# Optimization experiments

Hardware: AMD Instinct MI355X
Metric: run time of the kernel (lower is better)

## Reference

```python
import jax, jax.numpy as jnp
import numpy as np

EPS = 1e-8


def _conv1d(x, w, b):
    # x: [B, E, L], w: [F, E, K], b: [F] -> [B, F, L] (k=3, pad=1 keeps length)
    y = jax.lax.conv_general_dilated(
        x, w, window_strides=(1,), padding=[(1, 1)],
        dimension_numbers=("NCH", "OIH", "NCH"))
    return y + b[None, :, None]


def setup_inputs() -> dict:
    key = jax.random.key(0)
    kq, ka, ke, kw, kb, ku = jax.random.split(key, 6)
    B, QL, AL = 512, 128, 512
    V, E, F, K = 50000, 300, 400, 3
    question = jax.random.randint(kq, (B, QL), 0, V + 1, dtype=jnp.int64)
    answer = jax.random.randint(ka, (B, AL), 0, V + 1, dtype=jnp.int64)
    emb_table = jax.random.normal(ke, (V + 1, E), dtype=jnp.float32)
    emb_table = emb_table.at[0].set(0.0)  # padding_idx=0
    conv_w = jax.random.normal(kw, (F, E, K), dtype=jnp.float32) * 0.05
    conv_b = jax.random.normal(kb, (F,), dtype=jnp.float32) * 0.05
    U = jax.random.normal(ku, (F, F), dtype=jnp.float32) * 0.1
    return {"question": question, "answer": answer, "emb_table": emb_table,
            "conv_w": conv_w, "conv_b": conv_b, "U": U}


def reference(question, answer, emb_table, conv_w, conv_b, U):
    q = emb_table[question]              # [B, QL, E]
    a = emb_table[answer]                # [B, AL, E]
    Q = _conv1d(q.transpose(0, 2, 1), conv_w, conv_b)   # [B, F, QL]
    A = _conv1d(a.transpose(0, 2, 1), conv_w, conv_b)   # [B, F, AL]
    # G = tanh(Q^T U A): [B, QL, AL]
    G = jnp.tanh(jnp.einsum("bfq,fg,bga->bqa", Q, U, A))
    roQ = jax.nn.softmax(jnp.max(G, axis=2), axis=1)    # [B, QL]
    roA = jax.nn.softmax(jnp.max(G, axis=1), axis=1)    # [B, AL]
    rQ = jnp.einsum("bfq,bq->bf", Q, roQ)               # [B, F]
    rA = jnp.einsum("bfa,ba->bf", A, roA)               # [B, F]
    nQ = jnp.maximum(jnp.linalg.norm(rQ, axis=1), EPS)
    nA = jnp.maximum(jnp.linalg.norm(rA, axis=1), EPS)
    return jnp.sum(rQ * rA, axis=1) / (nQ * nA)         # [B]
```

## Files before the change

kernel.cpp:

```cpp
#include <hip/hip_runtime.h>
#include <math.h>

typedef unsigned int   uint32;
typedef unsigned short ushort16;
typedef __attribute__((ext_vector_type(8))) short  short8;
typedef __attribute__((ext_vector_type(4))) float  floatx4;

#define Bb   512
#define QLn  128
#define ALn  512
#define En   300
#define Fn   400
#define OW   416
#define EPAD 320
#define NV   50001
#define ECROWS 50176
#define ECSTRIDE 2560

typedef const __attribute__((address_space(1))) unsigned int guint_t;
typedef __attribute__((address_space(3))) unsigned int luint_t;
#define GLDS16(g, l) __builtin_amdgcn_global_load_lds((guint_t*)(g), (luint_t*)(l), 16, 0, 0)

static __device__ __forceinline__ float bf_lo(uint32 u) { return __uint_as_float(u << 16); }
static __device__ __forceinline__ float bf_hi(uint32 u) { return __uint_as_float(u & 0xffff0000u); }
static __device__ __forceinline__ ushort16 f2bf(float f) {
    uint32 u = __float_as_uint(f);
    uint32 r = (u + 0x7fffu + ((u >> 16) & 1u)) >> 16;
    return (ushort16)r;
}
static __device__ __forceinline__ uint32 pack2(float a, float b) {
    return (uint32)f2bf(a) | ((uint32)f2bf(b) << 16);
}

__global__ __launch_bounds__(128) void embcvt_kernel(
        const float* __restrict__ emb, char* __restrict__ embbf)
{
    const int r = blockIdx.x, j = threadIdx.x;
    const float* er = emb + (size_t)r * En;
    uint32* orow = (uint32*)(embbf + (size_t)r * 640);
    for (int d = j; d < 160; d += 128) {
        uint32 v = 0;
        if (d < 150) {
            float2 f2v = *(const float2*)(er + 2 * d);
            v = pack2(f2v.x, f2v.y);
        }
        orow[d] = v;
    }
}

__global__ __launch_bounds__(256) void prep_wt(
        const float* __restrict__ W, const float* __restrict__ cb,
        ushort16* __restrict__ Wt2, float* __restrict__ bias2)
{
    const int f = blockIdx.x, t = threadIdx.x;
    for (int p2 = t; p2 < 480; p2 += 256) {
        int p = 2 * p2;
        float v0 = 0.f, v1 = 0.f;
        if (f < Fn) {
            int kk = p / EPAD, e = p - kk * EPAD;
            if (e < En)     v0 = W[(size_t)f * 900 + e * 3 + kk];
            if (e + 1 < En) v1 = W[(size_t)f * 900 + (e + 1) * 3 + kk];
        }
        *(uint32*)&Wt2[(size_t)f * 960 + p] = pack2(v0, v1);
    }
    if (t == 0) bias2[f] = (f < Fn) ? cb[f] : 0.f;
}

__global__ __launch_bounds__(256) void prep_ub(
        const float* __restrict__ U, ushort16* __restrict__ Ub)
{
    const int g = blockIdx.x, t = threadIdx.x;
    uint32* orow = (uint32*)(Ub + (size_t)g * 416);
    for (int f2 = t; f2 < 208; f2 += 256) {
        int f = 2 * f2;
        float v0 = 0.f, v1 = 0.f;
        if (g < Fn) {
            if (f < Fn)     v0 = U[(size_t)f * Fn + g];
            if (f + 1 < Fn) v1 = U[(size_t)(f + 1) * Fn + g];
        }
        orow[f2] = pack2(v0, v1);
    }
}

__global__ __launch_bounds__(512) void ec_gemm(
        const char* __restrict__ embbf, const char* __restrict__ Wt2,
        char* __restrict__ EC)
{
    __shared__ __align__(16) char As[32768];
    __shared__ __align__(16) char Bs[32768];
    const int t = threadIdx.x, lane = t & 63, w = t >> 6;
    const int v0 = blockIdx.x * 256, c0 = blockIdx.y * 256;
    const int wr = w >> 2, wc = w & 3;
    const int fm = lane & 15;
    const int cg = ((lane & 3) - ((lane >> 3) & 3)) & 3;
    const int rl = lane >> 2;
    const int chunkOff = (((lane >> 4) + (fm >> 1)) & 3) * 16;

    const char* srcA[2];
    const char* srcB[2];
#pragma unroll
    for (int i = 0; i < 2; ++i) {
        srcA[i] = embbf + (size_t)(v0 + w * 32 + i * 16 + rl) * 640 + cg * 16;
        int n = c0 + w * 32 + i * 16 + rl;
        int kk = n / 416, f = n - kk * 416;
        if (n >= 1248) { kk = 0; f = 508; }
        srcB[i] = Wt2 + (size_t)f * 1920 + kk * 640 + cg * 16;
    }
    char* AsW = As + w * 2048;
    char* BsW = Bs + w * 2048;

    floatx4 acc[8][4];
    const floatx4 zz = {0.f, 0.f, 0.f, 0.f};
#pragma unroll
    for (int m = 0; m < 8; ++m)
#pragma unroll
        for (int n = 0; n < 4; ++n) acc[m][n] = zz;

#define ESTG(ko, buf) do {                                                    \
        const int _ko = (ko); const int _bo = (buf) * 16384;                  \
        GLDS16(srcA[0] + _ko, AsW + _bo);                                     \
        GLDS16(srcA[1] + _ko, AsW + _bo + 1024);                              \
        GLDS16(srcB[0] + _ko, BsW + _bo);                                     \
        GLDS16(srcB[1] + _ko, BsW + _bo + 1024);                              \
    } while (0)

    int cur = 0;
    ESTG(0, 0);
    __syncthreads();
    for (int ks = 0; ks < 10; ++ks) {
        const int nxt = cur ^ 1;
        if (ks < 9) ESTG((ks + 1) * 64, nxt);
        short8 af[8], bfv[4];
        const char* Ac = As + cur * 16384;
        const char* Bc = Bs + cur * 16384;
#pragma unroll
        for (int m = 0; m < 8; ++m)
            af[m] = *(const short8*)(Ac + (wr * 128 + m * 16 + fm) * 64 + chunkOff);
#pragma unroll
        for (int n = 0; n < 4; ++n)
            bfv[n] = *(const short8*)(Bc + (wc * 64 + n * 16 + fm) * 64 + chunkOff);
        __builtin_amdgcn_s_setprio(1);
#pragma unroll
        for (int m = 0; m < 8; ++m)
#pragma unroll
            for (int n = 0; n < 4; ++n)
                acc[m][n] = __builtin_amdgcn_mfma_f32_16x16x32_bf16(
                    bfv[n], af[m], acc[m][n], 0, 0, 0);
        __builtin_amdgcn_s_setprio(0);
        __syncthreads();
        cur = nxt;
    }
#undef ESTG

#pragma unroll
    for (int m = 0; m < 8; ++m) {
        const int v = v0 + wr * 128 + m * 16 + fm;
#pragma unroll
        for (int n = 0; n < 4; ++n) {
            const int f0 = c0 + wc * 64 + n * 16 + ((lane >> 4) * 4);
            uint2 o;
            o.x = pack2(acc[m][n][0], acc[m][n][1]);
            o.y = pack2(acc[m][n][2], acc[m][n][3]);
            *(uint2*)(EC + (size_t)v * ECSTRIDE + f0 * 2) = o;
        }
    }
}

static __device__ __forceinline__ void gather_one(
        const int* __restrict__ toks, const char* __restrict__ EC,
        const float* __restrict__ bias2, char* __restrict__ outb,
        int id, int L)
{
    const uint32 uid = (uint32)id;
    const int c = (int)(uid % 52u);
    const int r = (int)(uid / 52u);
    const int l = r & (L - 1), b = r / L;
    const int* tr = toks + (size_t)b * L;
    const int t0 = (l > 0)     ? tr[l - 1] : 0;
    const int t1 = tr[l];
    const int t2 = (l < L - 1) ? tr[l + 1] : 0;
    const uint4 x0 = *(const uint4*)(EC + (size_t)t0 * ECSTRIDE +        c * 16);
    const uint4 x1 = *(const uint4*)(EC + (size_t)t1 * ECSTRIDE +  832 + c * 16);
    const uint4 x2 = *(const uint4*)(EC + (size_t)t2 * ECSTRIDE + 1664 + c * 16);
    const float4 b0 = *(const float4*)(bias2 + c * 8);
    const float4 b1 = *(const float4*)(bias2 + c * 8 + 4);
    uint4 o;
    o.x = pack2(bf_lo(x0.x) + bf_lo(x1.x) + bf_lo(x2.x) + b0.x,
                bf_hi(x0.x) + bf_hi(x1.x) + bf_hi(x2.x) + b0.y);
    o.y = pack2(bf_lo(x0.y) + bf_lo(x1.y) + bf_lo(x2.y) + b0.z,
                bf_hi(x0.y) + bf_hi(x1.y) + bf_hi(x2.y) + b0.w);
    o.z = pack2(bf_lo(x0.z) + bf_lo(x1.z) + bf_lo(x2.z) + b1.x,
                bf_hi(x0.z) + bf_hi(x1.z) + bf_hi(x2.z) + b1.y);
    o.w = pack2(bf_lo(x0.w) + bf_lo(x1.w) + bf_lo(x2.w) + b1.z,
                bf_hi(x0.w) + bf_hi(x1.w) + bf_hi(x2.w) + b1.w);
    *(uint4*)(outb + (size_t)r * 832 + c * 16) = o;
}

#define GQB 1024
#define GAB 4096
__global__ __launch_bounds__(256) void gather_both(
        const int* __restrict__ question, const int* __restrict__ answer,
        const char* __restrict__ EC, const float* __restrict__ bias2,
        char* __restrict__ qb, char* __restrict__ ab, int nb)
{
    const int bx = blockIdx.x, t = threadIdx.x;
    if (bx < GQB) {
        const int total = nb * QLn * 52;
        for (int id = bx * 256 + t; id < total; id += GQB * 256)
            gather_one(question, EC, bias2, qb, id, QLn);
    } else {
        const int total = nb * ALn * 52;
        for (int id = (bx - GQB) * 256 + t; id < total; id += GAB * 256)
            gather_one(answer, EC, bias2, ab, id, ALn);
    }
}

template<int NWM, int NWN, int MF, int NF, int BR>
static __device__ __forceinline__ void qp_tile(
        const char* __restrict__ Qb, const char* __restrict__ Ub,
        char* __restrict__ ob, int col0, char* As, char* Bs)
{
    const int t = threadIdx.x, lane = t & 63, w = t >> 6;
    const int wr = w / NWN, wc = w % NWN;
    const int fm = lane & 15;
    const int cg = ((lane & 3) - ((lane >> 3) & 3)) & 3;
    const int rl = lane >> 2;
    const int chunkOff = (((lane >> 4) + (fm >> 1)) & 3) * 16;

    const char* srcA = Qb + (size_t)(w * 16 + rl) * 832 + cg * 16;
    const char* srcB0; const char* srcB1 = 0;
    if (BR == 256) {
        srcB0 = Ub + (size_t)(col0 + w * 32 + rl) * 832 + cg * 16;
        srcB1 = srcB0 + (size_t)16 * 832;
    } else {
        srcB0 = Ub + (size_t)(col0 + w * 16 + rl) * 832 + cg * 16;
        srcB1 = Ub + (size_t)(col0 + 128 + w * 16 + rl) * 832 + cg * 16;
    }
    char* AsW = As + w * 1024;
    char* BsW0; char* BsW1;
    if (BR == 256) { BsW0 = Bs + w * 2048; BsW1 = BsW0 + 1024; }
    else           { BsW0 = Bs + w * 1024; BsW1 = Bs + 8192 + w * 1024; }
    const int BUFB = BR * 64;

    floatx4 acc[MF][NF];
    const floatx4 zz = {0.f, 0.f, 0.f, 0.f};
#pragma unroll
    for (int m = 0; m < MF; ++m)
#pragma unroll
        for (int n = 0; n < NF; ++n) acc[m][n] = zz;

#define QSTG(ko, buf) do {                                                    \
        const int _ko = (ko);                                                 \
        GLDS16(srcA + _ko, AsW + (buf) * 8192);                               \
        GLDS16(srcB0 + _ko, BsW0 + (buf) * BUFB);                             \
        if (BR == 256 || w < 2) GLDS16(srcB1 + _ko, BsW1 + (buf) * BUFB);     \
    } while (0)

    int cur = 0;
    QSTG(0, 0);
    __syncthreads();
    for (int ks = 0; ks < 13; ++ks) {
        const int nxt = cur ^ 1;
        if (ks < 12) QSTG((ks + 1) * 64, nxt);
        short8 af[MF], bfv[NF];
        const char* Ac = As + cur * 8192;
        const char* Bc = Bs + cur * BUFB;
#pragma unroll
        for (int m = 0; m < MF; ++m)
            af[m] = *(const short8*)(Ac + (wr * (MF * 16) + m * 16 + fm) * 64 + chunkOff);
#pragma unroll
        for (int n = 0; n < NF; ++n)
            bfv[n] = *(const short8*)(Bc + (wc * (NF * 16) + n * 16 + fm) * 64 + chunkOff);
        __builtin_amdgcn_s_setprio(1);
#pragma unroll
        for (int m = 0; m < MF; ++m)
#pragma unroll
            for (int n = 0; n < NF; ++n)
                acc[m][n] = __builtin_amdgcn_mfma_f32_16x16x32_bf16(
                    af[m], bfv[n], acc[m][n], 0, 0, 0);
        __builtin_amdgcn_s_setprio(0);
        __syncthreads();
        cur = nxt;
    }
#undef QSTG

#pragma unroll
    for (int m = 0; m < MF; ++m) {
        const int row = wr * (MF * 16) + m * 16 + ((lane >> 4) * 4);
#pragma unroll
        for (int n = 0; n < NF; ++n) {
            const int col = col0 + wc * (NF * 16) + n * 16 + fm;
#pragma unroll
            for (int r = 0; r < 4; ++r)
                *(ushort16*)(ob + (size_t)(row + r) * 832 + col * 2) =
                    f2bf(acc[m][n][r]);
        }
    }
}

__global__ __launch_bounds__(512) void qp_gemm(
        const char* __restrict__ qb, const char* __restrict__ Ub,
        char* __restrict__ qpb, int nb)
{
    __shared__ __align__(16) char As[16384];
    __shared__ __align__(16) char Bs[32768];
    const int bx = blockIdx.x;
    const int xcd = bx & 7, rest = bx >> 3;
    const int nt = rest & 1, b = (rest >> 1) * 8 + xcd;
    if (b >= nb) return;
    const char* Qb = qb + (size_t)b * 106496;
    char* ob = qpb + (size_t)b * 106496;
    if (nt == 0)
        qp_tile<2, 4, 4, 4, 256>(Qb, Ub, ob, 0, As, Bs);
    else
        qp_tile<4, 2, 2, 5, 160>(Qb, Ub, ob, 256, As, Bs);
}

__global__ __launch_bounds__(256) void fused_g(
        const ushort16* __restrict__ Qp,
        const ushort16* __restrict__ Av,
        float* __restrict__ rowPart,
        float* __restrict__ colMg,
        int nb)
{
    __shared__ __align__(16) char Qs[16384];
    __shared__ __align__(16) char Asl[32768];
    __shared__ float rowM4[128][4];

    const int t = threadIdx.x, lane = t & 63, w = t >> 6;
    const int bx = blockIdx.x;
    const int xcd = bx & 7, rest = bx >> 3;
    const int c = rest & 1, b = (rest >> 1) * 8 + xcd;
    if (b >= nb) return;
    const int fm = lane & 15;
    const int cg = ((lane & 3) - ((lane >> 3) & 3)) & 3;
    const int rl = lane >> 2;
    const int chunkOff = (((lane >> 4) + (fm >> 1)) & 3) * 16;

    const char* Qpb = (const char*)Qp + (size_t)b * 106496;
    const char* Ab  = (const char*)Av + (size_t)b * 425984 + (size_t)c * 212992;
    const char* srcQ0 = Qpb + (size_t)(w * 16 + rl) * 832 + cg * 16;
    const char* srcQ1 = Qpb + (size_t)(64 + w * 16 + rl) * 832 + cg * 16;
    const char* srcA0 = Ab  + (size_t)(w * 64 + rl) * 832 + cg * 16;

    floatx4 acc[8][4];
    const floatx4 zz = {0.f, 0.f, 0.f, 0.f};
#pragma unroll
    for (int m = 0; m < 8; ++m)
#pragma unroll
        for (int n = 0; n < 4; ++n) acc[m][n] = zz;

#define FSTG(ko, buf) do {                                                    \
        const int _ko = (ko);                                                 \
        GLDS16(srcQ0 + _ko, Qs + (buf) * 8192 + w * 1024);                    \
        GLDS16(srcQ1 + _ko, Qs + (buf) * 8192 + 4096 + w * 1024);             \
        GLDS16(srcA0 + _ko,         Asl + (buf) * 16384 + w * 4096);          \
        GLDS16(srcA0 + 13312 + _ko, Asl + (buf) * 16384 + w * 4096 + 1024);   \
        GLDS16(srcA0 + 26624 + _ko, Asl + (buf) * 16384 + w * 4096 + 2048);   \
        GLDS16(srcA0 + 39936 + _ko, Asl + (buf) * 16384 + w * 4096 + 3072);   \
    } while (0)

    int cur = 0;
    FSTG(0, 0);
    __syncthreads();

    for (int ks = 0; ks < 13; ++ks) {
        const int nxt = cur ^ 1;
        if (ks < 12) FSTG((ks + 1) * 64, nxt);

        short8 qa[8], aa_[4];
        const char* Qc = Qs + cur * 8192;
        const char* Ac = Asl + cur * 16384;
#pragma unroll
        for (int m = 0; m < 8; ++m)
            qa[m] = *(const short8*)(Qc + (m * 16 + fm) * 64 + chunkOff);
#pragma unroll
        for (int n = 0; n < 4; ++n)
            aa_[n] = *(const short8*)(Ac + (w * 64 + n * 16 + fm) * 64 + chunkOff);
        __builtin_amdgcn_s_setprio(1);
#pragma unroll
        for (int m = 0; m < 8; ++m)
#pragma unroll
            for (int n = 0; n < 4; ++n)
                acc[m][n] = __builtin_amdgcn_mfma_f32_16x16x32_bf16(
                    qa[m], aa_[n], acc[m][n], 0, 0, 0);
        __builtin_amdgcn_s_setprio(0);
        __syncthreads();
        cur = nxt;
    }
#undef FSTG

#pragma unroll
    for (int m = 0; m < 8; ++m)
#pragma unroll
        for (int r = 0; r < 4; ++r) {
            float v = fmaxf(fmaxf(acc[m][0][r], acc[m][1][r]),
                            fmaxf(acc[m][2][r], acc[m][3][r]));
            v = fmaxf(v, __shfl_xor(v, 1));
            v = fmaxf(v, __shfl_xor(v, 2));
            v = fmaxf(v, __shfl_xor(v, 4));
            v = fmaxf(v, __shfl_xor(v, 8));
            if (fm == 0) rowM4[m * 16 + (lane >> 4) * 4 + r][w] = v;
        }
#pragma unroll
    for (int n = 0; n < 4; ++n) {
        float v = -1e30f;
#pragma unroll
        for (int m = 0; m < 8; ++m)
#pragma unroll
            for (int r = 0; r < 4; ++r) v = fmaxf(v, acc[m][n][r]);
        v = fmaxf(v, __shfl_xor(v, 16));
        v = fmaxf(v, __shfl_xor(v, 32));
        if (lane < 16)
            colMg[(size_t)b * 512 + c * 256 + w * 64 + n * 16 + lane] = v;
    }
    __syncthreads();
    if (t < 128)
        rowPart[((size_t)b * 2 + c) * 128 + t] =
            fmaxf(fmaxf(rowM4[t][0], rowM4[t][1]),
                  fmaxf(rowM4[t][2], rowM4[t][3]));
}

static __device__ __forceinline__ float block_reduce_max_1k(float v, volatile float* red) {
    int t = threadIdx.x;
    red[t] = v; __syncthreads();
    for (int s = 512; s > 0; s >>= 1) {
        if (t < s) red[t] = fmaxf(red[t], red[t + s]);
        __syncthreads();
    }
    float r = red[0]; __syncthreads();
    return r;
}
static __device__ __forceinline__ float block_reduce_sum_1k(float v, volatile float* red) {
    int t = threadIdx.x;
    red[t] = v; __syncthreads();
    for (int s = 512; s > 0; s >>= 1) {
        if (t < s) red[t] = red[t] + red[t + s];
        __syncthreads();
    }
    float r = red[0]; __syncthreads();
    return r;
}

__global__ __launch_bounds__(1024) void fused_pool(
        const ushort16* __restrict__ Qv,
        const ushort16* __restrict__ Av,
        const float* __restrict__ rowPart,
        const float* __restrict__ colMg,
        float* __restrict__ out)
{
    __shared__ float colv[ALn];
    __shared__ float roq[QLn];
    __shared__ float red[1024];
    __shared__ float part[4][4][208];
    const int t = threadIdx.x, b = blockIdx.x;

    float v = -1e30f;
    if (t < QLn) {
        const float* rp = rowPart + (size_t)b * 256;
        v = tanhf(fmaxf(rp[t], rp[128 + t]));
    }
    float vmax = block_reduce_max_1k(v, red);
    float ex = (t < QLn) ? __expf(v - vmax) : 0.f;
    float ssum = block_reduce_sum_1k(ex, red);
    if (t < QLn) roq[t] = ex / ssum;

    float cv = (t < ALn) ? tanhf(colMg[(size_t)b * 512 + t]) : -1e30f;
    float cmax = block_reduce_max_1k(cv, red);
    float e0 = (t < ALn) ? __expf(cv - cmax) : 0.f;
    float csum = block_reduce_sum_1k(e0, red);
    if (t < ALn) colv[t] = e0 / csum;
    __syncthreads();

    if (t < 832) {
        const int h = t / 208, c = t - h * 208;
        float rq0 = 0.f, rq1 = 0.f, ra0 = 0.f, ra1 = 0.f;
        const uint32* Qb32 = (const uint32*)((const char*)Qv + (size_t)b * 106496);
#pragma unroll 4
        for (int q = h * 32; q < h * 32 + 32; ++q) {
            float wv = roq[q];
            uint32 u = Qb32[q * 208 + c];
            rq0 = fmaf(bf_lo(u), wv, rq0);
            rq1 = fmaf(bf_hi(u), wv, rq1);
        }
        const uint32* Ab32 = (const uint32*)((const char*)Av + (size_t)b * 425984);
#pragma unroll 4
        for (int a = h * 128; a < h * 128 + 128; ++a) {
            float wv = colv[a];
            uint32 u = Ab32[a * 208 + c];
            ra0 = fmaf(bf_lo(u), wv, ra0);
            ra1 = fmaf(bf_hi(u), wv, ra1);
        }
        part[0][h][c] = rq0; part[1][h][c] = rq1;
        part[2][h][c] = ra0; part[3][h][c] = ra1;
    }
    __syncthreads();

    float dd = 0.f, qq = 0.f, aam = 0.f;
    if (t < 208) {
        float q0 = part[0][0][t] + part[0][1][t] + part[0][2][t] + part[0][3][t];
        float q1 = part[1][0][t] + part[1][1][t] + part[1][2][t] + part[1][3][t];
        float a0 = part[2][0][t] + part[2][1][t] + part[2][2][t] + part[2][3][t];
        float a1 = part[3][0][t] + part[3][1][t] + part[3][2][t] + part[3][3][t];
        dd  = q0 * a0 + q1 * a1;
        qq  = q0 * q0 + q1 * q1;
        aam = a0 * a0 + a1 * a1;
    }
    dd  = block_reduce_sum_1k(dd, red);
    qq  = block_reduce_sum_1k(qq, red);
    aam = block_reduce_sum_1k(aam, red);
    if (t == 0) {
        float nq = fmaxf(sqrtf(qq), 1e-8f);
        float na = fmaxf(sqrtf(aam), 1e-8f);
        out[b] = dd / (nq * na);
    }
}

extern "C" void kernel_launch(void* const* d_in, const int* in_sizes, int n_in,
                              void* d_out, int out_size, void* d_ws, size_t ws_size,
                              hipStream_t stream)
{
    const int*   question = (const int*)d_in[0];
    const int*   answer   = (const int*)d_in[1];
    const float* emb      = (const float*)d_in[2];
    const float* conv_w   = (const float*)d_in[3];
    const float* conv_b   = (const float*)d_in[4];
    const float* U        = (const float*)d_in[5];
    float* out = (float*)d_out;
    char* ws = (char*)d_ws;

    const size_t WT2B   = (size_t)512 * 960 * 2;
    const size_t UBB    = (size_t)416 * 416 * 2;
    const size_t ECB    = (size_t)ECROWS * ECSTRIDE;
    const size_t FIXED0 = WT2B + 2048 + UBB + ECB;
    const size_t QB     = (size_t)QLn * OW * 2;
    const size_t AB     = (size_t)ALn * OW * 2;
    const size_t MXB    = 4096;
    const size_t PER_B  = 2 * QB + AB + MXB;

    size_t avail = (ws_size > FIXED0) ? (ws_size - FIXED0) : 0;
    int CB = (int)(avail / PER_B);
    if (CB > Bb) CB = Bb;
    if (CB < 1)  CB = 1;
    int nch = (Bb + CB - 1) / CB;
    int CBe = (Bb + nch - 1) / nch;

    char*  wt2   = ws;
    float* bias2 = (float*)(ws + WT2B);
    char*  ub    = ws + WT2B + 2048;
    char*  EC    = ws + WT2B + 2048 + UBB;
    char*  embbf = ws + FIXED0;
    char*  qb    = ws + FIXED0;
    char*  qpb   = qb  + (size_t)CB * QB;
    char*  ab    = qpb + (size_t)CB * QB;
    float* rowP  = (float*)(ab + (size_t)CB * AB);
    float* colM  = rowP + (size_t)CB * 512;

    embcvt_kernel<<<NV, 128, 0, stream>>>(emb, embbf);
    prep_wt<<<512, 256, 0, stream>>>(conv_w, conv_b, (ushort16*)wt2, bias2);
    prep_ub<<<416, 256, 0, stream>>>(U, (ushort16*)ub);
    ec_gemm<<<dim3(196, 5), 512, 0, stream>>>(embbf, wt2, EC);

    for (int b0 = 0; b0 < Bb; b0 += CBe) {
        int nb = (Bb - b0 < CBe) ? (Bb - b0) : CBe;
        int nb8 = (nb + 7) / 8;
        gather_both<<<GQB + GAB, 256, 0, stream>>>(
            question + (size_t)b0 * QLn, answer + (size_t)b0 * ALn,
            EC, bias2, qb, ab, nb);
        qp_gemm<<<nb8 * 16, 512, 0, stream>>>(qb, ub, qpb, nb);
        fused_g<<<nb8 * 16, 256, 0, stream>>>((const ushort16*)qpb, (const ushort16*)ab,
                                              rowP, colM, nb);
        fused_pool<<<nb, 1024, 0, stream>>>((const ushort16*)qb, (const ushort16*)ab,
                                            rowP, colM, out + b0);
    }
}
```

Baseline: 614.9 us.

## Split fused_g rows and pooling across more blocks, transpose ec_gemm output

fused_g now splits the 128 question rows into two halves per block, doubling the grid and halving the accumulator registers. This should raise occupancy, at the cost of an extra column-max partial that pool_a has to merge. The 1024-thread pool kernel is replaced by a 512-thread pool_a that runs four blocks per batch, plus a small pool_b that combines their partial sums through a scratch buffer. ec_gemm swaps its MFMA operand order and writes the output as scattered 2-byte stores instead of packed 8-byte stores, which may cost store efficiency.

```diff
diff --git a/kernel.cpp b/kernel.cpp
--- a/kernel.cpp
+++ b/kernel.cpp
@@ -145,7 +145,7 @@
 #pragma unroll
             for (int n = 0; n < 4; ++n)
                 acc[m][n] = __builtin_amdgcn_mfma_f32_16x16x32_bf16(
-                    bfv[n], af[m], acc[m][n], 0, 0, 0);
+                    af[m], bfv[n], acc[m][n], 0, 0, 0);
         __builtin_amdgcn_s_setprio(0);
         __syncthreads();
         cur = nxt;
@@ -154,14 +154,14 @@
 
 #pragma unroll
     for (int m = 0; m < 8; ++m) {
-        const int v = v0 + wr * 128 + m * 16 + fm;
+        const int v = v0 + wr * 128 + m * 16 + ((lane >> 4) * 4);
 #pragma unroll
         for (int n = 0; n < 4; ++n) {
-            const int f0 = c0 + wc * 64 + n * 16 + ((lane >> 4) * 4);
-            uint2 o;
-            o.x = pack2(acc[m][n][0], acc[m][n][1]);
-            o.y = pack2(acc[m][n][2], acc[m][n][3]);
-            *(uint2*)(EC + (size_t)v * ECSTRIDE + f0 * 2) = o;
+            const int col = c0 + wc * 64 + n * 16 + fm;
+#pragma unroll
+            for (int r = 0; r < 4; ++r)
+                *(ushort16*)(EC + (size_t)(v + r) * ECSTRIDE + col * 2) =
+                    f2bf(acc[m][n][r]);
         }
     }
 }
@@ -323,37 +323,35 @@
         float* __restrict__ colMg,
         int nb)
 {
-    __shared__ __align__(16) char Qs[16384];
+    __shared__ __align__(16) char Qs[8192];
     __shared__ __align__(16) char Asl[32768];
-    __shared__ float rowM4[128][4];
+    __shared__ float rowM4[64][4];
 
     const int t = threadIdx.x, lane = t & 63, w = t >> 6;
     const int bx = blockIdx.x;
     const int xcd = bx & 7, rest = bx >> 3;
-    const int c = rest & 1, b = (rest >> 1) * 8 + xcd;
+    const int c = rest & 1, mh = (rest >> 1) & 1, b = (rest >> 2) * 8 + xcd;
     if (b >= nb) return;
     const int fm = lane & 15;
     const int cg = ((lane & 3) - ((lane >> 3) & 3)) & 3;
     const int rl = lane >> 2;
     const int chunkOff = (((lane >> 4) + (fm >> 1)) & 3) * 16;
 
-    const char* Qpb = (const char*)Qp + (size_t)b * 106496;
+    const char* Qpb = (const char*)Qp + (size_t)b * 106496 + (size_t)mh * 64 * 832;
     const char* Ab  = (const char*)Av + (size_t)b * 425984 + (size_t)c * 212992;
-    const char* srcQ0 = Qpb + (size_t)(w * 16 + rl) * 832 + cg * 16;
-    const char* srcQ1 = Qpb + (size_t)(64 + w * 16 + rl) * 832 + cg * 16;
+    const char* srcQ  = Qpb + (size_t)(w * 16 + rl) * 832 + cg * 16;
     const char* srcA0 = Ab  + (size_t)(w * 64 + rl) * 832 + cg * 16;
 
-    floatx4 acc[8][4];
+    floatx4 acc[4][4];
     const floatx4 zz = {0.f, 0.f, 0.f, 0.f};
 #pragma unroll
-    for (int m = 0; m < 8; ++m)
+    for (int m = 0; m < 4; ++m)
 #pragma unroll
         for (int n = 0; n < 4; ++n) acc[m][n] = zz;
 
 #define FSTG(ko, buf) do {                                                    \
         const int _ko = (ko);                                                 \
-        GLDS16(srcQ0 + _ko, Qs + (buf) * 8192 + w * 1024);                    \
-        GLDS16(srcQ1 + _ko, Qs + (buf) * 8192 + 4096 + w * 1024);             \
+        GLDS16(srcQ + _ko,          Qs  + (buf) * 4096  + w * 1024);          \
         GLDS16(srcA0 + _ko,         Asl + (buf) * 16384 + w * 4096);          \
         GLDS16(srcA0 + 13312 + _ko, Asl + (buf) * 16384 + w * 4096 + 1024);   \
         GLDS16(srcA0 + 26624 + _ko, Asl + (buf) * 16384 + w * 4096 + 2048);   \
@@ -368,18 +366,18 @@
         const int nxt = cur ^ 1;
         if (ks < 12) FSTG((ks + 1) * 64, nxt);
 
-        short8 qa[8], aa_[4];
-        const char* Qc = Qs + cur * 8192;
+        short8 qa[4], aa_[4];
+        const char* Qc = Qs + cur * 4096;
         const char* Ac = Asl + cur * 16384;
 #pragma unroll
-        for (int m = 0; m < 8; ++m)
+        for (int m = 0; m < 4; ++m)
             qa[m] = *(const short8*)(Qc + (m * 16 + fm) * 64 + chunkOff);
 #pragma unroll
         for (int n = 0; n < 4; ++n)
             aa_[n] = *(const short8*)(Ac + (w * 64 + n * 16 + fm) * 64 + chunkOff);
         __builtin_amdgcn_s_setprio(1);
 #pragma unroll
-        for (int m = 0; m < 8; ++m)
+        for (int m = 0; m < 4; ++m)
 #pragma unroll
             for (int n = 0; n < 4; ++n)
                 acc[m][n] = __builtin_amdgcn_mfma_f32_16x16x32_bf16(
@@ -391,7 +389,7 @@
 #undef FSTG
 
 #pragma unroll
-    for (int m = 0; m < 8; ++m)
+    for (int m = 0; m < 4; ++m)
 #pragma unroll
         for (int r = 0; r < 4; ++r) {
             float v = fmaxf(fmaxf(acc[m][0][r], acc[m][1][r]),
@@ -406,35 +404,35 @@
     for (int n = 0; n < 4; ++n) {
         float v = -1e30f;
 #pragma unroll
-        for (int m = 0; m < 8; ++m)
+        for (int m = 0; m < 4; ++m)
 #pragma unroll
             for (int r = 0; r < 4; ++r) v = fmaxf(v, acc[m][n][r]);
         v = fmaxf(v, __shfl_xor(v, 16));
         v = fmaxf(v, __shfl_xor(v, 32));
         if (lane < 16)
-            colMg[(size_t)b * 512 + c * 256 + w * 64 + n * 16 + lane] = v;
+            colMg[((size_t)b * 2 + mh) * 512 + c * 256 + w * 64 + n * 16 + lane] = v;
     }
     __syncthreads();
-    if (t < 128)
-        rowPart[((size_t)b * 2 + c) * 128 + t] =
+    if (t < 64)
+        rowPart[((size_t)b * 2 + c) * 128 + mh * 64 + t] =
             fmaxf(fmaxf(rowM4[t][0], rowM4[t][1]),
                   fmaxf(rowM4[t][2], rowM4[t][3]));
 }
 
-static __device__ __forceinline__ float block_reduce_max_1k(float v, volatile float* red) {
+static __device__ __forceinline__ float red_max_512(float v, volatile float* red) {
     int t = threadIdx.x;
     red[t] = v; __syncthreads();
-    for (int s = 512; s > 0; s >>= 1) {
+    for (int s = 256; s > 0; s >>= 1) {
         if (t < s) red[t] = fmaxf(red[t], red[t + s]);
         __syncthreads();
     }
     float r = red[0]; __syncthreads();
     return r;
 }
-static __device__ __forceinline__ float block_reduce_sum_1k(float v, volatile float* red) {
+static __device__ __forceinline__ float red_sum_512(float v, volatile float* red) {
     int t = threadIdx.x;
     red[t] = v; __syncthreads();
-    for (int s = 512; s > 0; s >>= 1) {
+    for (int s = 256; s > 0; s >>= 1) {
         if (t < s) red[t] = red[t] + red[t + s];
         __syncthreads();
     }
@@ -442,73 +440,106 @@
     return r;
 }
 
-__global__ __launch_bounds__(1024) void fused_pool(
+__global__ __launch_bounds__(512) void pool_a(
         const ushort16* __restrict__ Qv,
         const ushort16* __restrict__ Av,
         const float* __restrict__ rowPart,
         const float* __restrict__ colMg,
-        float* __restrict__ out)
+        float* __restrict__ scratch,
+        int nb)
 {
     __shared__ float colv[ALn];
     __shared__ float roq[QLn];
-    __shared__ float red[1024];
-    __shared__ float part[4][4][208];
-    const int t = threadIdx.x, b = blockIdx.x;
+    __shared__ float red[512];
+    __shared__ float part[2][4][208];
+    const int t = threadIdx.x, bx = blockIdx.x;
+    const int qtr = bx & 3, b = bx >> 2;
 
     float v = -1e30f;
     if (t < QLn) {
         const float* rp = rowPart + (size_t)b * 256;
         v = tanhf(fmaxf(rp[t], rp[128 + t]));
     }
-    float vmax = block_reduce_max_1k(v, red);
+    float vmax = red_max_512(v, red);
     float ex = (t < QLn) ? __expf(v - vmax) : 0.f;
-    float ssum = block_reduce_sum_1k(ex, red);
+    float ssum = red_sum_512(ex, red);
     if (t < QLn) roq[t] = ex / ssum;
 
-    float cv = (t < ALn) ? tanhf(colMg[(size_t)b * 512 + t]) : -1e30f;
-    float cmax = block_reduce_max_1k(cv, red);
-    float e0 = (t < ALn) ? __expf(cv - cmax) : 0.f;
-    float csum = block_reduce_sum_1k(e0, red);
-    if (t < ALn) colv[t] = e0 / csum;
+    const float* cm = colMg + (size_t)b * 1024;
+    float cv = tanhf(fmaxf(cm[t], cm[512 + t]));
+    float cmax = red_max_512(cv, red);
+    float e0 = __expf(cv - cmax);
+    float csum = red_sum_512(e0, red);
+    colv[t] = e0 / csum;
     __syncthreads();
 
-    if (t < 832) {
-        const int h = t / 208, c = t - h * 208;
+    if (t < 416) {
+        const int half = t / 208, c = t - half * 208;
         float rq0 = 0.f, rq1 = 0.f, ra0 = 0.f, ra1 = 0.f;
         const uint32* Qb32 = (const uint32*)((const char*)Qv + (size_t)b * 106496);
+        const int q0r = qtr * 32 + half * 16;
 #pragma unroll 4
-        for (int q = h * 32; q < h * 32 + 32; ++q) {
+        for (int q = q0r; q < q0r + 16; ++q) {
             float wv = roq[q];
             uint32 u = Qb32[q * 208 + c];
             rq0 = fmaf(bf_lo(u), wv, rq0);
             rq1 = fmaf(bf_hi(u), wv, rq1);
         }
         const uint32* Ab32 = (const uint32*)((const char*)Av + (size_t)b * 425984);
+        const int a0r = qtr * 128 + half * 64;
 #pragma unroll 4
-        for (int a = h * 128; a < h * 128 + 128; ++a) {
+        for (int a = a0r; a < a0r + 64; ++a) {
             float wv = colv[a];
             uint32 u = Ab32[a * 208 + c];
             ra0 = fmaf(bf_lo(u), wv, ra0);
             ra1 = fmaf(bf_hi(u), wv, ra1);
         }
-        part[0][h][c] = rq0; part[1][h][c] = rq1;
-        part[2][h][c] = ra0; part[3][h][c] = ra1;
+        part[half][0][c] = rq0; part[half][1][c] = rq1;
+        part[half][2][c] = ra0; part[half][3][c] = ra1;
     }
     __syncthreads();
 
+    if (t < 208) {
+        float* sc = scratch + ((size_t)b * 4 + qtr) * 832;
+        sc[t]       = part[0][0][t] + part[1][0][t];
+        sc[208 + t] = part[0][1][t] + part[1][1][t];
+        sc[416 + t] = part[0][2][t] + part[1][2][t];
+        sc[624 + t] = part[0][3][t] + part[1][3][t];
+    }
+}
+
+static __device__ __forceinline__ float red_sum_256(float v, volatile float* red) {
+    int t = threadIdx.x;
+    red[t] = v; __syncthreads();
+    for (int s = 128; s > 0; s >>= 1) {
+        if (t < s) red[t] = red[t] + red[t + s];
+        __syncthreads();
+    }
+    float r = red[0]; __syncthreads();
+    return r;
+}
+
+__global__ __launch_bounds__(256) void pool_b(
+        const float* __restrict__ scratch, float* __restrict__ out, int nb)
+{
+    __shared__ float red[256];
+    const int t = threadIdx.x, b = blockIdx.x;
     float dd = 0.f, qq = 0.f, aam = 0.f;
     if (t < 208) {
-        float q0 = part[0][0][t] + part[0][1][t] + part[0][2][t] + part[0][3][t];
-        float q1 = part[1][0][t] + part[1][1][t] + part[1][2][t] + part[1][3][t];
-        float a0 = part[2][0][t] + part[2][1][t] + part[2][2][t] + part[2][3][t];
-        float a1 = part[3][0][t] + part[3][1][t] + part[3][2][t] + part[3][3][t];
+        float q0 = 0.f, q1 = 0.f, a0 = 0.f, a1 = 0.f;
+#pragma unroll
+        for (int qtr = 0; qtr < 4; ++qtr) {
+            const float* sc = scratch + ((size_t)b * 4 + qtr) * 832;
+            q0 += sc[t]; q1 += sc[208 + t];
+            a0 += sc[416 + t]; a1 += sc[624 + t];
+        }
         dd  = q0 * a0 + q1 * a1;
         qq  = q0 * q0 + q1 * q1;
         aam = a0 * a0 + a1 * a1;
     }
-    dd  = block_reduce_sum_1k(dd, red);
-    qq  = block_reduce_sum_1k(qq, red);
-    aam = block_reduce_sum_1k(aam, red);
+    dd  = red_sum_256(dd, red);
+    qq  = red_sum_256(qq, red);
+    aam = red_sum_256(aam, red);
     if (t == 0) {
         float nq = fmaxf(sqrtf(qq), 1e-8f);
         float na = fmaxf(sqrtf(aam), 1e-8f);
@@ -535,7 +566,7 @@
     const size_t FIXED0 = WT2B + 2048 + UBB + ECB;
     const size_t QB     = (size_t)QLn * OW * 2;
     const size_t AB     = (size_t)ALn * OW * 2;
-    const size_t MXB    = 4096;
+    const size_t MXB    = 20480;
     const size_t PER_B  = 2 * QB + AB + MXB;
 
     size_t avail = (ws_size > FIXED0) ? (ws_size - FIXED0) : 0;
@@ -554,7 +585,8 @@
     char*  qpb   = qb  + (size_t)CB * QB;
     char*  ab    = qpb + (size_t)CB * QB;
     float* rowP  = (float*)(ab + (size_t)CB * AB);
-    float* colM  = rowP + (size_t)CB * 512;
+    float* colM  = rowP + (size_t)CB * 256;
+    float* scr   = colM + (size_t)CB * 1024;
 
     embcvt_kernel<<<NV, 128, 0, stream>>>(emb, embbf);
     prep_wt<<<512, 256, 0, stream>>>(conv_w, conv_b, (ushort16*)wt2, bias2);
@@ -568,9 +600,10 @@
             question + (size_t)b0 * QLn, answer + (size_t)b0 * ALn,
             EC, bias2, qb, ab, nb);
         qp_gemm<<<nb8 * 16, 512, 0, stream>>>(qb, ub, qpb, nb);
-        fused_g<<<nb8 * 16, 256, 0, stream>>>((const ushort16*)qpb, (const ushort16*)ab,
+        fused_g<<<nb8 * 32, 256, 0, stream>>>((const ushort16*)qpb, (const ushort16*)ab,
                                               rowP, colM, nb);
-        fused_pool<<<nb, 1024, 0, stream>>>((const ushort16*)qb, (const ushort16*)ab,
-                                            rowP, colM, out + b0);
-    }
-}
+        pool_a<<<nb * 4, 512, 0, stream>>>((const ushort16*)qb, (const ushort16*)ab,
+                                           rowP, colM, scr, nb);
+        pool_b<<<nb, 256, 0, stream>>>(scr, out + b0, nb);
+    }
+}
```

Result: faster. 568.0 us (-7.6%).
